# Kernel optimization log

Hardware: AMD Instinct MI355X
Metric: run time of the kernel (lower is better)

The kernel has to match this reference:

```python
import jax, jax.numpy as jnp
import numpy as np

WEIGHT0 = 1.0
WEIGHT1 = 1.0
GAMMA = 2.0
N = 33554432  # number of flattened per-pixel predictions
EPS = 1e-6    # keep probabilities strictly inside (0,1) so log is finite


def setup_inputs() -> dict:
    key = jax.random.key(0)
    k1, k2 = jax.random.split(key)
    u = jax.random.uniform(k1, (N,), dtype=jnp.float32)
    inp = u * (1.0 - 2.0 * EPS) + EPS  # probabilities in (eps, 1-eps)
    tgt = jax.random.randint(k2, (N,), 0, 2, dtype=jnp.int32)
    return {"input": inp, "target": tgt}


def reference(input, target):
    # Faithful vectorized form of the per-element Python loop:
    #   t==1: log(p)   * |1-p|^gamma * w1
    #   else: log(1-p) * |p|^gamma   * w0
    # summed, negated, divided by N.
    pos = jnp.log(input) * jnp.abs(1.0 - input) ** GAMMA * WEIGHT1
    neg = jnp.log(1.0 - input) * jnp.abs(input) ** GAMMA * WEIGHT0
    per_el = jnp.where(target == 1, pos, neg)
    return -jnp.mean(per_el)
```

## Files before the change

### kernel.cpp

```cpp
#include <hip/hip_runtime.h>


constexpr int   N_TOTAL = 33554432;
constexpr float NEG_INV_N = -1.0f / 33554432.0f;

__global__ __launch_bounds__(256) void focal_loss_kernel(
    const float4* __restrict__ inp,
    const int4*  __restrict__ tgt,
    float* __restrict__ out,
    int n_vec)
{
    int tid    = blockIdx.x * blockDim.x + threadIdx.x;
    int stride = gridDim.x * blockDim.x;

    float acc = 0.0f;
    for (int i = tid; i < n_vec; i += stride) {
        float4 p4 = inp[i];
        int4   t4 = tgt[i];
        float p[4] = {p4.x, p4.y, p4.z, p4.w};
        int   t[4] = {t4.x, t4.y, t4.z, t4.w};
#pragma unroll
        for (int j = 0; j < 4; ++j) {
            float s = (t[j] == 1) ? p[j] : (1.0f - p[j]);
            float q = 1.0f - s;
            acc += __logf(s) * q * q;
        }
    }

#pragma unroll
    for (int off = 32; off > 0; off >>= 1)
        acc += __shfl_down(acc, off, 64);

    __shared__ float ws[4];
    int lane = threadIdx.x & 63;
    int wave = threadIdx.x >> 6;
    if (lane == 0) ws[wave] = acc;
    __syncthreads();

    if (threadIdx.x == 0) {
        float b = ws[0] + ws[1] + ws[2] + ws[3];
        atomicAdd(out, b * NEG_INV_N);
    }
}

extern "C" void kernel_launch(void* const* d_in, const int* in_sizes, int n_in,
                              void* d_out, int out_size, void* d_ws, size_t ws_size,
                              hipStream_t stream) {
    const float4* inp = (const float4*)d_in[0];
    const int4*   tgt = (const int4*)d_in[1];
    float*        out = (float*)d_out;

    int n_vec = N_TOTAL / 4;

    hipMemsetAsync(d_out, 0, sizeof(float), stream);

    focal_loss_kernel<<<2048, 256, 0, stream>>>(inp, tgt, out, n_vec);
}
```

Baseline: 282.4 us.

## Use blocked contiguous indexing with 4x unrolled loads and two-pass reduction

Each block now works on a contiguous chunk with a compile-time trip count. The loop is unrolled by four so eight 16-byte loads are in flight per thread before any compute. The memset and the atomicAdd are replaced by per-block partials written to workspace and summed by a second single-block kernel, which also gives a deterministic result. The intent is more memory-level parallelism and less launch and atomic overhead, at the cost of an extra kernel launch and hardcoded sizes.

```diff
diff --git a/kernel.cpp b/kernel.cpp
--- a/kernel.cpp
+++ b/kernel.cpp
@@ -1,46 +1,84 @@
 #include <hip/hip_runtime.h>
 
 
-constexpr int   N_TOTAL = 33554432;
+constexpr int   N_TOTAL   = 33554432;
+constexpr int   N_VEC     = N_TOTAL / 4;
+constexpr int   BLOCKS    = 2048;
+constexpr int   THREADS   = 256;
+constexpr int   VEC_PER_BLOCK = N_VEC / BLOCKS;
+constexpr int   ITERS     = VEC_PER_BLOCK / THREADS;
 constexpr float NEG_INV_N = -1.0f / 33554432.0f;
 
-__global__ __launch_bounds__(256) void focal_loss_kernel(
+__device__ __forceinline__ float focal_term(float p, int t) {
+    float s = (t == 1) ? p : (1.0f - p);
+    float q = 1.0f - s;
+    return __logf(s) * q * q;
+}
+
+__global__ __launch_bounds__(THREADS) void focal_partial_kernel(
     const float4* __restrict__ inp,
     const int4*  __restrict__ tgt,
-    float* __restrict__ out,
-    int n_vec)
+    float* __restrict__ partials)
 {
-    int tid    = blockIdx.x * blockDim.x + threadIdx.x;
-    int stride = gridDim.x * blockDim.x;
+    const int base = blockIdx.x * VEC_PER_BLOCK + threadIdx.x;
 
     float acc = 0.0f;
-    for (int i = tid; i < n_vec; i += stride) {
-        float4 p4 = inp[i];
-        int4   t4 = tgt[i];
-        float p[4] = {p4.x, p4.y, p4.z, p4.w};
-        int   t[4] = {t4.x, t4.y, t4.z, t4.w};
 #pragma unroll
-        for (int j = 0; j < 4; ++j) {
-            float s = (t[j] == 1) ? p[j] : (1.0f - p[j]);
-            float q = 1.0f - s;
-            acc += __logf(s) * q * q;
-        }
+    for (int it = 0; it < ITERS; it += 4) {
+        float4 p0 = inp[base + (it + 0) * THREADS];
+        float4 p1 = inp[base + (it + 1) * THREADS];
+        float4 p2 = inp[base + (it + 2) * THREADS];
+        float4 p3 = inp[base + (it + 3) * THREADS];
+        int4   t0 = tgt[base + (it + 0) * THREADS];
+        int4   t1 = tgt[base + (it + 1) * THREADS];
+        int4   t2 = tgt[base + (it + 2) * THREADS];
+        int4   t3 = tgt[base + (it + 3) * THREADS];
+
+        acc += focal_term(p0.x, t0.x) + focal_term(p0.y, t0.y)
+             + focal_term(p0.z, t0.z) + focal_term(p0.w, t0.w);
+        acc += focal_term(p1.x, t1.x) + focal_term(p1.y, t1.y)
+             + focal_term(p1.z, t1.z) + focal_term(p1.w, t1.w);
+        acc += focal_term(p2.x, t2.x) + focal_term(p2.y, t2.y)
+             + focal_term(p2.z, t2.z) + focal_term(p2.w, t2.w);
+        acc += focal_term(p3.x, t3.x) + focal_term(p3.y, t3.y)
+             + focal_term(p3.z, t3.z) + focal_term(p3.w, t3.w);
     }
 
 #pragma unroll
     for (int off = 32; off > 0; off >>= 1)
         acc += __shfl_down(acc, off, 64);
 
-    __shared__ float ws[4];
+    __shared__ float ws[THREADS / 64];
     int lane = threadIdx.x & 63;
     int wave = threadIdx.x >> 6;
     if (lane == 0) ws[wave] = acc;
     __syncthreads();
 
-    if (threadIdx.x == 0) {
-        float b = ws[0] + ws[1] + ws[2] + ws[3];
-        atomicAdd(out, b * NEG_INV_N);
-    }
+    if (threadIdx.x == 0)
+        partials[blockIdx.x] = ws[0] + ws[1] + ws[2] + ws[3];
+}
+
+__global__ __launch_bounds__(THREADS) void focal_final_kernel(
+    const float* __restrict__ partials,
+    float* __restrict__ out)
+{
+    float acc = 0.0f;
+#pragma unroll
+    for (int k = 0; k < BLOCKS / THREADS; ++k)
+        acc += partials[k * THREADS + threadIdx.x];
+
+#pragma unroll
+    for (int off = 32; off > 0; off >>= 1)
+        acc += __shfl_down(acc, off, 64);
+
+    __shared__ float ws[THREADS / 64];
+    int lane = threadIdx.x & 63;
+    int wave = threadIdx.x >> 6;
+    if (lane == 0) ws[wave] = acc;
+    __syncthreads();
+
+    if (threadIdx.x == 0)
+        out[0] = (ws[0] + ws[1] + ws[2] + ws[3]) * NEG_INV_N;
 }
 
 extern "C" void kernel_launch(void* const* d_in, const int* in_sizes, int n_in,
@@ -49,10 +87,8 @@
     const float4* inp = (const float4*)d_in[0];
     const int4*   tgt = (const int4*)d_in[1];
     float*        out = (float*)d_out;
+    float*        partials = (float*)d_ws;
 
-    int n_vec = N_TOTAL / 4;
-
-    hipMemsetAsync(d_out, 0, sizeof(float), stream);
-
-    focal_loss_kernel<<<2048, 256, 0, stream>>>(inp, tgt, out, n_vec);
+    focal_partial_kernel<<<BLOCKS, THREADS, 0, stream>>>(inp, tgt, partials);
+    focal_final_kernel<<<1, THREADS, 0, stream>>>(partials, out);
 }
```

Measured after the change: 277.2 us. Within noise of the previous version (-1.8%).
